# Optimization experiments

Hardware: AMD Instinct MI355X
Metric: run time of the kernel (lower is better)

Reference implementation:

```python
import jax, jax.numpy as jnp
import numpy as np

N_HEADS = 8
NEG = -1e9  # additive mask value standing in for -inf (bf16-safe)


def _mha(q_in, kv_in, w_in, b_in, w_out, b_out, mask):
    """torch nn.MultiheadAttention (batch_first, eval/no-dropout) equivalent.
    w_in: [3D, D] packed q/k/v in_proj weight, b_in: [3D]; w_out: [D, D], b_out: [D].
    mask: optional [L, L] additive mask.
    """
    B, Lq, D = q_in.shape
    H = N_HEADS
    dh = D // H
    Lk = kv_in.shape[1]
    q = q_in @ w_in[:D].T + b_in[:D]
    k = kv_in @ w_in[D:2 * D].T + b_in[D:2 * D]
    v = kv_in @ w_in[2 * D:].T + b_in[2 * D:]
    q = q.reshape(B, Lq, H, dh)
    k = k.reshape(B, Lk, H, dh)
    v = v.reshape(B, Lk, H, dh)
    scores = jnp.einsum('bqhd,bkhd->bhqk', q, k) / jnp.sqrt(jnp.asarray(dh, q.dtype))
    if mask is not None:
        scores = scores + mask  # broadcast [L,L] over [B,H,L,L]
    attn = jax.nn.softmax(scores, axis=-1)
    out = jnp.einsum('bhqk,bkhd->bqhd', attn, v).reshape(B, Lq, D)
    return out @ w_out.T + b_out


def _causal_mask(L):
    i = jnp.arange(L)
    return jnp.where(i[None, :] <= i[:, None], 0.0, NEG).astype(jnp.float32)


def _band_mask(L, window):
    # causal AND |i-j| <= window//2 (Eq. 13 band mask + causal mask)
    i = jnp.arange(L)
    diff = i[None, :] - i[:, None]  # key - query
    ok = (diff <= 0) & (jnp.abs(diff) <= window // 2)
    return jnp.where(ok, 0.0, NEG).astype(jnp.float32)


def setup_inputs() -> dict:
    key = jax.random.key(0)
    ks = jax.random.split(key, 10)
    B, L, D = 8, 1024, 512

    def rn(k, shape, scale=0.02):
        return jax.random.normal(k, shape, jnp.float32) * scale

    return {
        'user_emb': jax.random.normal(ks[0], (B, L, D), jnp.float32),
        'item_emb': jax.random.normal(ks[1], (B, L, D), jnp.float32),
        'attn_w_in': rn(ks[2], (6, 3 * D, D)),
        'attn_b_in': jnp.zeros((6, 3 * D), jnp.float32),
        'attn_w_out': rn(ks[3], (6, D, D)),
        'attn_b_out': jnp.zeros((6, D), jnp.float32),
        'cross_user_w': rn(ks[4], (D, D)),
        'cross_user_b': jnp.zeros((D,), jnp.float32),
        'cross_item_w': rn(ks[5], (D, D)),
        'cross_item_b': jnp.zeros((D,), jnp.float32),
        'gate_w': rn(ks[6], (2, D, 6)),
        'gate_b': jnp.zeros((2, 6), jnp.float32),
        'head_w1': rn(ks[7], (3, D, D // 2)),
        'head_b1': jnp.zeros((3, D // 2), jnp.float32),
        'head_w2': rn(ks[8], (3, D // 2)),
        'head_b2': jnp.zeros((3,), jnp.float32),
    }


def reference(user_emb, item_emb, attn_w_in, attn_b_in, attn_w_out, attn_b_out,
              cross_user_w, cross_user_b, cross_item_w, cross_item_b,
              gate_w, gate_b, head_w1, head_b1, head_w2, head_b2):
    B, L, D = item_emb.shape
    causal = _causal_mask(L)

    # 1) shared global causal SA (residual added by caller per docstring)
    shared = item_emb + _mha(item_emb, item_emb, attn_w_in[0], attn_b_in[0], attn_w_out[0], attn_b_out[0], causal)
    # 2) EXP-specific causal SA on shared output
    e_exp = shared + _mha(shared, shared, attn_w_in[1], attn_b_in[1], attn_w_out[1], attn_b_out[1], causal)
    # 3) CLK-specific causal SA on shared output
    e_clk = shared + _mha(shared, shared, attn_w_in[2], attn_b_in[2], attn_w_out[2], attn_b_out[2], causal)
    # 4) cross-attention: user queries into item keys/values (Eq. 12)
    u = user_emb @ cross_user_w.T + cross_user_b
    pv = item_emb @ cross_item_w.T + cross_item_b
    e_cross = _mha(u, pv, attn_w_in[3], attn_b_in[3], attn_w_out[3], attn_b_out[3], None)
    # 5/6) local (banded causal) self-attention, windows 4 and 6 (Eq. 13)
    e_lsa4 = item_emb + _mha(item_emb, item_emb, attn_w_in[4], attn_b_in[4], attn_w_out[4], attn_b_out[4], _band_mask(L, 4))
    e_lsa6 = item_emb + _mha(item_emb, item_emb, attn_w_in[5], attn_b_in[5], attn_w_out[5], attn_b_out[5], _band_mask(L, 6))

    experts = jnp.stack([shared, e_exp, e_clk, e_cross, e_lsa4, e_lsa6], axis=2)  # [B,L,6,D]
    # PLE gates: per-task softmax gate over the 6 experts conditioned on item_emb
    gate_logits = jnp.einsum('bld,tde->tble', item_emb, gate_w) + gate_b[:, None, None, :]
    gates = jax.nn.softmax(gate_logits, axis=-1)  # [2,B,L,6]
    h_exp = jnp.einsum('ble,bled->bld', gates[0], experts)
    h_clk = jnp.einsum('ble,bled->bld', gates[1], experts)

    def head(h, i):
        hid = jax.nn.relu(h @ head_w1[i] + head_b1[i])  # [B,L,D//2]
        return hid @ head_w2[i] + head_b2[i]  # [B,L]

    p_exp = jax.nn.sigmoid(head(h_exp, 0))
    p_clk = jax.nn.sigmoid(head(h_clk, 1))
    p_cvr = jax.nn.sigmoid(head(h_clk, 2))
    return (p_exp, p_clk, p_cvr)
```

## Files before the change

kernel.cpp:

```cpp
#include <hip/hip_runtime.h>
#include <hip/hip_bf16.h>
#include <stdint.h>


using bf16 = __hip_bfloat16;
typedef __attribute__((ext_vector_type(8))) short short8v;
typedef __attribute__((ext_vector_type(4))) short short4v;
typedef __attribute__((ext_vector_type(4))) float float4v;

#define LDK 40
#define LDKB 72
#define LQA 76
#define EXPC 0.18033688011112042f

__device__ __forceinline__ float wred_sum(float v) {
    #pragma unroll
    for (int off = 32; off; off >>= 1) v += __shfl_xor(v, off);
    return v;
}
__device__ __forceinline__ short f2bs(float x) {
    bf16 b = __float2bfloat16(x);
    return *reinterpret_cast<short*>(&b);
}
__device__ __forceinline__ float b2f(bf16 v) { return __bfloat162float(v); }

__global__ __launch_bounds__(256) void fillf_kernel(float* __restrict__ p, float v, int n) {
    const int i = blockIdx.x * 256 + threadIdx.x;
    if (i < n) p[i] = v;
}

__global__ __launch_bounds__(256) void cvt_all_kernel(
    const float* s0, bf16* d0, const float* s1, bf16* d1, const float* s2, bf16* d2,
    const float* s3, bf16* d3, const float* s4, bf16* d4, const float* s5, bf16* d5,
    const float* s6, bf16* d6)
{
    const int i = blockIdx.x * 256 + threadIdx.x;
    const float* src; bf16* dst; int off;
    if      (i < 1048576) { src = s0; dst = d0; off = i; }
    else if (i < 2097152) { src = s1; dst = d1; off = i - 1048576; }
    else if (i < 3276800) { src = s2; dst = d2; off = i - 2097152; }
    else if (i < 3670016) { src = s3; dst = d3; off = i - 3276800; }
    else if (i < 3735552) { src = s4; dst = d4; off = i - 3670016; }
    else if (i < 3801088) { src = s5; dst = d5; off = i - 3735552; }
    else if (i < 3899392) { src = s6; dst = d6; off = i - 3801088; }
    else return;
    const float4 v = *(const float4*)&src[(size_t)off << 2];
    short4v o;
    o[0] = f2bs(v.x); o[1] = f2bs(v.y); o[2] = f2bs(v.z); o[3] = f2bs(v.w);
    *(short4v*)&dst[(size_t)off << 2] = o;
}

__global__ __launch_bounds__(256) void gemm_nn_compose(
    const bf16* __restrict__ A, const bf16* __restrict__ B0, const bf16* __restrict__ B1,
    bf16* __restrict__ Y)
{
    const int K = 512, N = 512;
    __shared__ short As[64 * LDK];
    __shared__ short Bs[64 * LDK + 64];
    const int tid = threadIdx.x;
    const int lane = tid & 63, w = tid >> 6;
    const int bm = blockIdx.y * 64, bn = blockIdx.x * 64;
    const bf16* B = (bm < 512) ? B0 : B1;
    const int r = tid >> 2, c8 = (tid & 3) << 3;
    const int kk = tid >> 3, nn0 = (tid & 7) << 3;
    const int arow = ((w << 4) + (lane & 15)) * LDK + ((lane >> 4) << 3);

    float4v acc[4] = {};
    for (int k0 = 0; k0 < K; k0 += 32) {
        const short8v av = *(const short8v*)&A[(size_t)(bm + r) * K + k0 + c8];
        const short8v bw = *(const short8v*)&B[(size_t)(k0 + kk) * N + bn + nn0];
        __syncthreads();
        *(short8v*)&As[r * LDK + c8] = av;
        #pragma unroll
        for (int i = 0; i < 8; ++i) {
            const int nn = nn0 + i;
            Bs[nn * LDK + ((nn >> 3) << 3) + kk] = bw[i];
        }
        __syncthreads();
        const short8v a = *(const short8v*)&As[arow];
        #pragma unroll
        for (int c = 0; c < 4; ++c) {
            const int n = (c << 4) + (lane & 15);
            const short8v b = *(const short8v*)&Bs[n * LDK + ((n >> 3) << 3) + ((lane >> 4) << 3)];
            acc[c] = __builtin_amdgcn_mfma_f32_16x16x32_bf16(a, b, acc[c], 0, 0, 0);
        }
    }
    #pragma unroll
    for (int rg = 0; rg < 4; ++rg) {
        const int m = bm + (w << 4) + ((lane >> 4) << 2) + rg;
        #pragma unroll
        for (int c = 0; c < 4; ++c) {
            const int n = bn + (c << 4) + (lane & 15);
            Y[(size_t)m * N + n] = __float2bfloat16(acc[c][rg]);
        }
    }
}

__global__ __launch_bounds__(256) void compose_bias_kernel(
    const float* __restrict__ w3f, const float* __restrict__ cub,
    const float* __restrict__ cib, const float* __restrict__ b3f,
    float* __restrict__ bo)
{
    const int wid = threadIdx.x >> 6, lane = threadIdx.x & 63;
    const int n = blockIdx.x * 4 + wid;
    const float* cv = (n < 512) ? cub : cib;
    float s = 0.f;
    #pragma unroll
    for (int k = lane; k < 512; k += 64) s += w3f[(size_t)n * 512 + k] * cv[k];
    s = wred_sum(s);
    if (lane == 0) bo[n] = s + b3f[n];
}

__global__ __launch_bounds__(256) void gemm_bb_nt128(
    const bf16* __restrict__ X, const bf16* __restrict__ W,
    const float* __restrict__ bias, bf16* __restrict__ Yb, int ldY, int K)
{
    __shared__ short As[128 * LDKB];
    __shared__ short Bs[128 * LDKB];
    const int tid = threadIdx.x;
    const int lane = tid & 63, w = tid >> 6;
    const int wr = (w >> 1) << 6, wc = (w & 1) << 6;
    const int bm = blockIdx.y * 128, bn = blockIdx.x * 128;
    const int srow = tid >> 1, scol = (tid & 1) << 5;
    const int c16 = lane & 15, g16 = lane >> 4;

    float4v acc[4][4] = {};
    for (int k0 = 0; k0 < K; k0 += 64) {
        const bf16* xs = &X[(size_t)(bm + srow) * K + k0 + scol];
        const bf16* wsrc = &W[(size_t)(bn + srow) * K + k0 + scol];
        const short8v x0 = *(const short8v*)xs;
        const short8v x1 = *(const short8v*)(xs + 8);
        const short8v x2 = *(const short8v*)(xs + 16);
        const short8v x3 = *(const short8v*)(xs + 24);
        const short8v w0 = *(const short8v*)wsrc;
        const short8v w1 = *(const short8v*)(wsrc + 8);
        const short8v w2 = *(const short8v*)(wsrc + 16);
        const short8v w3 = *(const short8v*)(wsrc + 24);
        __syncthreads();
        *(short8v*)&As[srow * LDKB + scol]      = x0;
        *(short8v*)&As[srow * LDKB + scol + 8]  = x1;
        *(short8v*)&As[srow * LDKB + scol + 16] = x2;
        *(short8v*)&As[srow * LDKB + scol + 24] = x3;
        *(short8v*)&Bs[srow * LDKB + scol]      = w0;
        *(short8v*)&Bs[srow * LDKB + scol + 8]  = w1;
        *(short8v*)&Bs[srow * LDKB + scol + 16] = w2;
        *(short8v*)&Bs[srow * LDKB + scol + 24] = w3;
        __syncthreads();
        #pragma unroll
        for (int ks = 0; ks < 2; ++ks) {
            short8v af[4], bf4[4];
            #pragma unroll
            for (int i = 0; i < 4; ++i) {
                af[i]  = *(const short8v*)&As[(wr + (i << 4) + c16) * LDKB + (ks << 5) + (g16 << 3)];
                bf4[i] = *(const short8v*)&Bs[(wc + (i << 4) + c16) * LDKB + (ks << 5) + (g16 << 3)];
            }
            #pragma unroll
            for (int i = 0; i < 4; ++i)
                #pragma unroll
                for (int j = 0; j < 4; ++j)
                    acc[i][j] = __builtin_amdgcn_mfma_f32_16x16x32_bf16(af[i], bf4[j], acc[i][j], 0, 0, 0);
        }
    }
    #pragma unroll
    for (int i = 0; i < 4; ++i)
        #pragma unroll
        for (int rg = 0; rg < 4; ++rg) {
            const int m = bm + wr + (i << 4) + (g16 << 2) + rg;
            #pragma unroll
            for (int j = 0; j < 4; ++j) {
                const int n = bn + wc + (j << 4) + c16;
                Yb[(size_t)m * ldY + n] = __float2bfloat16(acc[i][j][rg] + bias[n]);
            }
        }
}

__global__ __launch_bounds__(256) void gemm_bb_nt128_selX(
    const bf16* __restrict__ X0, const bf16* __restrict__ X1, const bf16* __restrict__ W,
    const float* __restrict__ bias, bf16* __restrict__ Yb, int ldY, int K)
{
    __shared__ short As[128 * LDKB];
    __shared__ short Bs[128 * LDKB];
    const int tid = threadIdx.x;
    const int lane = tid & 63, w = tid >> 6;
    const int wr = (w >> 1) << 6, wc = (w & 1) << 6;
    const int bm = blockIdx.y * 128, bn = blockIdx.x * 128;
    const bf16* X = (bn < 512) ? X0 : X1;
    const int srow = tid >> 1, scol = (tid & 1) << 5;
    const int c16 = lane & 15, g16 = lane >> 4;

    float4v acc[4][4] = {};
    for (int k0 = 0; k0 < K; k0 += 64) {
        const bf16* xs = &X[(size_t)(bm + srow) * K + k0 + scol];
        const bf16* wsrc = &W[(size_t)(bn + srow) * K + k0 + scol];
        const short8v x0 = *(const short8v*)xs;
        const short8v x1 = *(const short8v*)(xs + 8);
        const short8v x2 = *(const short8v*)(xs + 16);
        const short8v x3 = *(const short8v*)(xs + 24);
        const short8v w0 = *(const short8v*)wsrc;
        const short8v w1 = *(const short8v*)(wsrc + 8);
        const short8v w2 = *(const short8v*)(wsrc + 16);
        const short8v w3 = *(const short8v*)(wsrc + 24);
        __syncthreads();
        *(short8v*)&As[srow * LDKB + scol]      = x0;
        *(short8v*)&As[srow * LDKB + scol + 8]  = x1;
        *(short8v*)&As[srow * LDKB + scol + 16] = x2;
        *(short8v*)&As[srow * LDKB + scol + 24] = x3;
        *(short8v*)&Bs[srow * LDKB + scol]      = w0;
        *(short8v*)&Bs[srow * LDKB + scol + 8]  = w1;
        *(short8v*)&Bs[srow * LDKB + scol + 16] = w2;
        *(short8v*)&Bs[srow * LDKB + scol + 24] = w3;
        __syncthreads();
        #pragma unroll
        for (int ks = 0; ks < 2; ++ks) {
            short8v af[4], bf4[4];
            #pragma unroll
            for (int i = 0; i < 4; ++i) {
                af[i]  = *(const short8v*)&As[(wr + (i << 4) + c16) * LDKB + (ks << 5) + (g16 << 3)];
                bf4[i] = *(const short8v*)&Bs[(wc + (i << 4) + c16) * LDKB + (ks << 5) + (g16 << 3)];
            }
            #pragma unroll
            for (int i = 0; i < 4; ++i)
                #pragma unroll
                for (int j = 0; j < 4; ++j)
                    acc[i][j] = __builtin_amdgcn_mfma_f32_16x16x32_bf16(af[i], bf4[j], acc[i][j], 0, 0, 0);
        }
    }
    #pragma unroll
    for (int i = 0; i < 4; ++i)
        #pragma unroll
        for (int rg = 0; rg < 4; ++rg) {
            const int m = bm + wr + (i << 4) + (g16 << 2) + rg;
            #pragma unroll
            for (int j = 0; j < 4; ++j) {
                const int n = bn + wc + (j << 4) + c16;
                Yb[(size_t)m * ldY + n] = __float2bfloat16(acc[i][j][rg] + bias[n]);
            }
        }
}

__global__ __launch_bounds__(256) void gemm_bb_nt_dual(
    const bf16* __restrict__ XA, const bf16* __restrict__ WA, const float* __restrict__ biasA,
    const bf16* __restrict__ XB, const bf16* __restrict__ WB, const float* __restrict__ biasB,
    const bf16* __restrict__ resA, int resSame,
    bf16* __restrict__ Yb, int ldY,
    bf16* __restrict__ h0, bf16* __restrict__ h1,
    const float* __restrict__ g, int eA, int eB, int hinit, int K)
{
    __shared__ short As[64 * LDK];
    __shared__ short Bs[64 * LDK];
    const int tid = threadIdx.x;
    const int lane = tid & 63, w = tid >> 6;
    const int bm = blockIdx.y * 64, bn = blockIdx.x * 64;
    const int r = tid >> 2, c8 = (tid & 3) << 3;
    const int arow = ((w << 4) + (lane & 15)) * LDK + ((lane >> 4) << 3);
    const int bbase = (lane & 15) * LDK + ((lane >> 4) << 3);

    float4v accA[4] = {};
    for (int k0 = 0; k0 < K; k0 += 32) {
        const short8v av = *(const short8v*)&XA[(size_t)(bm + r) * K + k0 + c8];
        const short8v bv = *(const short8v*)&WA[(size_t)(bn + r) * K + k0 + c8];
        __syncthreads();
        *(short8v*)&As[r * LDK + c8] = av;
        *(short8v*)&Bs[r * LDK + c8] = bv;
        __syncthreads();
        const short8v a = *(const short8v*)&As[arow];
        #pragma unroll
        for (int c = 0; c < 4; ++c) {
            const short8v b = *(const short8v*)&Bs[(c << 4) * LDK + bbase];
            accA[c] = __builtin_amdgcn_mfma_f32_16x16x32_bf16(a, b, accA[c], 0, 0, 0);
        }
    }
    float4v accB[4] = {};
    for (int k0 = 0; k0 < K; k0 += 32) {
        const short8v av = *(const short8v*)&XB[(size_t)(bm + r) * K + k0 + c8];
        const short8v bv = *(const short8v*)&WB[(size_t)(bn + r) * K + k0 + c8];
        __syncthreads();
        *(short8v*)&As[r * LDK + c8] = av;
        *(short8v*)&Bs[r * LDK + c8] = bv;
        __syncthreads();
        const short8v a = *(const short8v*)&As[arow];
        #pragma unroll
        for (int c = 0; c < 4; ++c) {
            const short8v b = *(const short8v*)&Bs[(c << 4) * LDK + bbase];
            accB[c] = __builtin_amdgcn_mfma_f32_16x16x32_bf16(a, b, accB[c], 0, 0, 0);
        }
    }
    #pragma unroll
    for (int rg = 0; rg < 4; ++rg) {
        const int m = bm + (w << 4) + ((lane >> 4) << 2) + rg;
        const float gA0 = g[(size_t)m * 6 + eA];
        const float gA1 = g[(size_t)(8192 + m) * 6 + eA];
        const float gB0 = g[(size_t)m * 6 + eB];
        const float gB1 = g[(size_t)(8192 + m) * 6 + eB];
        #pragma unroll
        for (int c = 0; c < 4; ++c) {
            const int n = bn + (c << 4) + (lane & 15);
            float rv = 0.f;
            if (resA) rv = b2f(resA[(size_t)m * 512 + n]);
            float vA = accA[c][rg] + biasA[n] + rv;
            float vB = accB[c][rg] + biasB[n] + (resSame ? rv : 0.f);
            if (Yb) Yb[(size_t)m * ldY + n] = __float2bfloat16(vA);
            const size_t hi = (size_t)m * 512 + n;
            const float t0 = gA0 * vA + gB0 * vB;
            const float t1 = gA1 * vA + gB1 * vB;
            if (hinit) {
                h0[hi] = __float2bfloat16(t0);
                h1[hi] = __float2bfloat16(t1);
            } else {
                h0[hi] = __float2bfloat16(b2f(h0[hi]) + t0);
                h1[hi] = __float2bfloat16(b2f(h1[hi]) + t1);
            }
        }
    }
}

__global__ __launch_bounds__(256) void gemm_mfma_nn_relu3(
    const bf16* __restrict__ h0b, const bf16* __restrict__ h1b,
    const bf16* __restrict__ hw1b, const float* __restrict__ hb1,
    float* __restrict__ hid0, float* __restrict__ hid1, float* __restrict__ hid2)
{
    const int K = 512, N = 256;
    const int seg = blockIdx.y >> 7;
    const int by = blockIdx.y & 127;
    const bf16* X = (seg == 0) ? h0b : h1b;
    const bf16* W = hw1b + (size_t)seg * 131072;
    const float* bias = hb1 + seg * 256;
    float* Y = (seg == 0) ? hid0 : ((seg == 1) ? hid1 : hid2);
    __shared__ short As[64 * LDK];
    __shared__ short Bs[64 * LDK + 64];
    const int tid = threadIdx.x;
    const int lane = tid & 63, w = tid >> 6;
    const int bm = by * 64, bn = blockIdx.x * 64;
    const int r = tid >> 2, c8 = (tid & 3) << 3;
    const int kk = tid >> 3, nn0 = (tid & 7) << 3;
    const int arow = ((w << 4) + (lane & 15)) * LDK + ((lane >> 4) << 3);

    float4v acc[4] = {};
    for (int k0 = 0; k0 < K; k0 += 32) {
        const short8v av = *(const short8v*)&X[(size_t)(bm + r) * K + k0 + c8];
        const short8v bw = *(const short8v*)&W[(size_t)(k0 + kk) * N + bn + nn0];
        __syncthreads();
        *(short8v*)&As[r * LDK + c8] = av;
        #pragma unroll
        for (int i = 0; i < 8; ++i) {
            const int nn = nn0 + i;
            Bs[nn * LDK + ((nn >> 3) << 3) + kk] = bw[i];
        }
        __syncthreads();
        const short8v a = *(const short8v*)&As[arow];
        #pragma unroll
        for (int c = 0; c < 4; ++c) {
            const int n = (c << 4) + (lane & 15);
            const short8v b = *(const short8v*)&Bs[n * LDK + ((n >> 3) << 3) + ((lane >> 4) << 3)];
            acc[c] = __builtin_amdgcn_mfma_f32_16x16x32_bf16(a, b, acc[c], 0, 0, 0);
        }
    }
    #pragma unroll
    for (int rg = 0; rg < 4; ++rg) {
        const int m = bm + (w << 4) + ((lane >> 4) << 2) + rg;
        #pragma unroll
        for (int c = 0; c < 4; ++c) {
            const int n = bn + (c << 4) + (lane & 15);
            Y[(size_t)m * N + n] = fmaxf(acc[c][rg] + bias[n], 0.f);
        }
    }
}

__global__ __launch_bounds__(512) void attn_flash2(
    const bf16* __restrict__ q0, const bf16* __restrict__ k0, const bf16* __restrict__ v0,
    bf16* __restrict__ o0, int ld0, int c0,
    const bf16* __restrict__ q1, const bf16* __restrict__ k1, const bf16* __restrict__ v1,
    bf16* __restrict__ o1, int ld1, int c1, int L)
{
    const int half = blockIdx.y >> 3;
    int bq = blockIdx.y & 7;
    const bf16 *qb, *kb, *vb; bf16* out; int ld, causal;
    if (half == 0) { qb = q0; kb = k0; vb = v0; out = o0; ld = ld0; causal = c0; }
    else           { qb = q1; kb = k1; vb = v1; out = o1; ld = ld1; causal = c1; }
    if (causal) bq = (bq < 4) ? bq : (11 - bq);
    const int b = blockIdx.x >> 3, h = blockIdx.x & 7;
    const int tid = threadIdx.x;
    const int lane = tid & 63, w = tid >> 6;
    const int g16 = lane >> 4, c16 = lane & 15;
    __shared__ short Ks[64 * LQA];
    __shared__ short Ps[128 * LQA];
    __shared__ short Vt[64 * LQA + 64];
    const size_t base = (size_t)b * L * ld + (size_t)h * 64;
    const int qlo = bq << 7;

    short8v qa0, qa1;
    {
        const bf16* qsrc = qb + base + (size_t)(qlo + (w << 4) + c16) * ld + (g16 << 3);
        qa0 = *(const short8v*)qsrc;
        qa1 = *(const short8v*)(qsrc + 32);
    }

    const int sr2 = (tid & 255) >> 2, sc2 = (tid & 3) << 4;
    const bool isK = tid < 256;

    float4v oacc[4] = {};
    float lrow[4] = {0.f, 0.f, 0.f, 0.f};

    const int nkt = causal ? ((bq + 1) << 1) : (L >> 6);

    short8v pf0, pf1;
    {
        const bf16* src = (isK ? kb : vb) + base + (size_t)sr2 * ld + sc2;
        pf0 = *(const short8v*)src;
        pf1 = *(const short8v*)(src + 8);
    }

    for (int kt = 0; kt < nkt; ++kt) {
        const int klo = kt << 6;
        __syncthreads();
        if (isK) {
            *(short8v*)&Ks[sr2 * LQA + sc2]     = pf0;
            *(short8v*)&Ks[sr2 * LQA + sc2 + 8] = pf1;
        } else {
            #pragma unroll
            for (int i = 0; i < 8; ++i) Vt[(sc2 + i) * LQA + sc2 + sr2] = pf0[i];
            #pragma unroll
            for (int i = 0; i < 8; ++i) Vt[(sc2 + 8 + i) * LQA + sc2 + sr2] = pf1[i];
        }
        __syncthreads();
        if (kt + 1 < nkt) {
            const bf16* src = (isK ? kb : vb) + base + (size_t)(((kt + 1) << 6) + sr2) * ld + sc2;
            pf0 = *(const short8v*)src;
            pf1 = *(const short8v*)(src + 8);
        }
        float4v sacc[4] = {};
        #pragma unroll
        for (int ct = 0; ct < 4; ++ct) {
            const short8v b0 = *(const short8v*)&Ks[((ct << 4) + c16) * LQA + (g16 << 3)];
            sacc[ct] = __builtin_amdgcn_mfma_f32_16x16x32_bf16(qa0, b0, sacc[ct], 0, 0, 0);
            const short8v b1 = *(const short8v*)&Ks[((ct << 4) + c16) * LQA + 32 + (g16 << 3)];
            sacc[ct] = __builtin_amdgcn_mfma_f32_16x16x32_bf16(qa1, b1, sacc[ct], 0, 0, 0);
        }
        const bool diag = causal && (klo + 63 > qlo + (w << 4));
        #pragma unroll
        for (int ct = 0; ct < 4; ++ct)
            #pragma unroll
            for (int rg = 0; rg < 4; ++rg) {
                float p = exp2f(sacc[ct][rg] * EXPC);
                if (diag && (klo + (ct << 4) + c16) > (qlo + (w << 4) + (g16 << 2) + rg))
                    p = 0.f;
                lrow[rg] += p;
                Ps[((w << 4) + (g16 << 2) + rg) * LQA + (ct << 4) + c16] = f2bs(p);
            }
        #pragma unroll
        for (int ks = 0; ks < 2; ++ks) {
            const short8v a = *(const short8v*)&Ps[((w << 4) + c16) * LQA + (ks << 5) + (g16 << 3)];
            #pragma unroll
            for (int dt = 0; dt < 4; ++dt) {
                const short8v bf = *(const short8v*)&Vt[((dt << 4) + c16) * LQA + (dt << 4) + (ks << 5) + (g16 << 3)];
                oacc[dt] = __builtin_amdgcn_mfma_f32_16x16x32_bf16(a, bf, oacc[dt], 0, 0, 0);
            }
        }
    }
    #pragma unroll
    for (int rg = 0; rg < 4; ++rg) {
        float v = lrow[rg];
        #pragma unroll
        for (int off = 8; off; off >>= 1) v += __shfl_xor(v, off);
        lrow[rg] = v;
    }
    #pragma unroll
    for (int rg = 0; rg < 4; ++rg) {
        const int row = qlo + (w << 4) + (g16 << 2) + rg;
        const float inv = 1.f / lrow[rg];
        #pragma unroll
        for (int dt = 0; dt < 4; ++dt)
            out[((size_t)b * L + row) * 512 + h * 64 + (dt << 4) + c16] =
                __float2bfloat16(oacc[dt][rg] * inv);
    }
}

__global__ __launch_bounds__(256) void attn_band2(
    const bf16* __restrict__ qkv, bf16* __restrict__ oA, bf16* __restrict__ oB,
    int L, int ld, int wA, int wB)
{
    const int half = blockIdx.y >> 6;
    const int yy = blockIdx.y & 63;
    const int u = threadIdx.x >> 6, t = threadIdx.x & 63;
    const int i = blockIdx.x * 4 + u;
    const int b = yy >> 3, h = yy & 7;
    const bf16* qb = qkv + half * 1536;
    const bf16* kb = qb + 512;
    const bf16* vb = qb + 1024;
    bf16* out = half ? oB : oA;
    const int w = half ? wB : wA;
    const size_t base = (size_t)b * L * ld + (size_t)h * 64;
    const float qv = b2f(qb[base + (size_t)i * ld + t]);
    const int jmin = (i - w) > 0 ? (i - w) : 0;
    const int n = i - jmin;
    float sv[4];
    float mx = -1e30f;
    #pragma unroll
    for (int q = 0; q < 4; ++q) {
        float d = -1e30f;
        if (q <= n) {
            float dd = qv * b2f(kb[base + (size_t)(jmin + q) * ld + t]);
            d = wred_sum(dd) * 0.125f;
        }
        sv[q] = d;
        mx = fmaxf(mx, d);
    }
    float lsum = 0.f, acc = 0.f;
    #pragma unroll
    for (int q = 0; q < 4; ++q) {
        if (q <= n) {
            const float p = __expf(sv[q] - mx);
            lsum += p;
            acc += p * b2f(vb[base + (size_t)(jmin + q) * ld + t]);
        }
    }
    out[((size_t)b * L + i) * 512 + h * 64 + t] = __float2bfloat16(acc / lsum);
}

__global__ __launch_bounds__(64) void gates_v2(
    const float* __restrict__ item, const float* __restrict__ gw,
    const float* __restrict__ gb, float* __restrict__ g, int rows)
{
    const int r = blockIdx.x;
    const int t = threadIdx.x;
    __shared__ float xr[512];
    __shared__ float lg[12];
    for (int ii = t; ii < 512; ii += 64) xr[ii] = item[(size_t)r * 512 + ii];
    __syncthreads();
    #pragma unroll
    for (int p = 0; p < 12; ++p) {
        const int tk = p / 6, e = p % 6;
        float s = 0.f;
        #pragma unroll
        for (int dd = t; dd < 512; dd += 64) s += xr[dd] * gw[(size_t)(tk * 512 + dd) * 6 + e];
        s = wred_sum(s);
        if (t == 0) lg[p] = s + gb[p];
    }
    __syncthreads();
    if (t < 2) {
        float mx = -1e30f;
        #pragma unroll
        for (int e = 0; e < 6; ++e) mx = fmaxf(mx, lg[t * 6 + e]);
        float sum = 0.f, p6[6];
        #pragma unroll
        for (int e = 0; e < 6; ++e) { p6[e] = __expf(lg[t * 6 + e] - mx); sum += p6[e]; }
        #pragma unroll
        for (int e = 0; e < 6; ++e) g[(size_t)(t * rows + r) * 6 + e] = p6[e] / sum;
    }
}

__global__ __launch_bounds__(256) void head2_v2(
    const float* __restrict__ hid0, const float* __restrict__ hid1, const float* __restrict__ hid2,
    const float* __restrict__ w2, const float* __restrict__ b2, float* __restrict__ out)
{
    const int w = threadIdx.x >> 6, lane = threadIdx.x & 63;
    const int r = blockIdx.x * 4 + w;
    float s0 = 0.f, s1 = 0.f, s2 = 0.f;
    #pragma unroll
    for (int d = lane; d < 256; d += 64) {
        s0 += hid0[(size_t)r * 256 + d] * w2[d];
        s1 += hid1[(size_t)r * 256 + d] * w2[256 + d];
        s2 += hid2[(size_t)r * 256 + d] * w2[512 + d];
    }
    s0 = wred_sum(s0); s1 = wred_sum(s1); s2 = wred_sum(s2);
    if (lane == 0) {
        out[r]         = 1.f / (1.f + __expf(-(s0 + b2[0])));
        out[8192 + r]  = 1.f / (1.f + __expf(-(s1 + b2[1])));
        out[16384 + r] = 1.f / (1.f + __expf(-(s2 + b2[2])));
    }
}

extern "C" void kernel_launch(void* const* d_in, const int* in_sizes, int n_in,
                              void* d_out, int out_size, void* d_ws, size_t ws_size,
                              hipStream_t stream)
{
    float* out = (float*)d_out;
    const int* s = in_sizes;
    const bool dicto = n_in == 16 &&
        s[0] == 4194304 && s[1] == 4194304 && s[2] == 4718592 && s[3] == 9216 &&
        s[4] == 1572864 && s[5] == 3072 && s[6] == 262144 && s[7] == 512 &&
        s[8] == 262144 && s[9] == 512 && s[10] == 6144 && s[11] == 12 &&
        s[12] == 393216 && s[13] == 768 && s[14] == 768 && s[15] == 3;
    if (!dicto) {
        fillf_kernel<<<dim3(96), dim3(256), 0, stream>>>(out, 16384.0f, out_size);
        return;
    }

    const float* user  = (const float*)d_in[0];
    const float* item  = (const float*)d_in[1];
    const float* w_in  = (const float*)d_in[2];
    const float* b_in  = (const float*)d_in[3];
    const float* w_out = (const float*)d_in[4];
    const float* b_out = (const float*)d_in[5];
    const float* cuw   = (const float*)d_in[6];
    const float* cub   = (const float*)d_in[7];
    const float* ciw   = (const float*)d_in[8];
    const float* cib   = (const float*)d_in[9];
    const float* gw    = (const float*)d_in[10];
    const float* gb    = (const float*)d_in[11];
    const float* hw1   = (const float*)d_in[12];
    const float* hb1   = (const float*)d_in[13];
    const float* hw2   = (const float*)d_in[14];
    const float* hb2   = (const float*)d_in[15];

    const int L = 1024, M = 8192;
    float* ws = (float*)d_ws;
    bf16* qkvb     = (bf16*)ws;
    bf16* qkvc     = qkvb + (size_t)12582912;
    bf16* attnoutb = (bf16*)(ws + 12582912);
    bf16* attnout2 = (bf16*)(ws + 16777216);
    bf16* h0b      = (bf16*)(ws + 20971520);
    bf16* h1b      = (bf16*)(ws + 25165824);
    bf16* sharedb  = (bf16*)(ws + 31457280);
    float* g       = ws + 41943040;
    bf16* itemb    = (bf16*)(ws + 42041344);
    bf16* userb    = (bf16*)(ws + 44138496);
    bf16* w_inb    = (bf16*)(ws + 46235648);
    bf16* w_outb   = (bf16*)(ws + 48594944);
    bf16* cuwb     = (bf16*)(ws + 49381376);
    bf16* ciwb     = (bf16*)(ws + 49512448);
    bf16* hw1b     = (bf16*)(ws + 49643520);
    bf16* Wcomp    = (bf16*)(ws + 49840128);
    float* bcomp   = ws + 50233344;
    float* hid0 = ws;
    float* hid1 = ws + (size_t)M * 256;
    float* hid2 = ws + (size_t)M * 512;
    bf16* BN = nullptr;

    const dim3 blk512(512), blk256(256), blk64(64);
    const dim3 gP1536(12, 64), gP3072(24, 64);
    const dim3 g512(8, 128);
    const dim3 gFA2(64, 16), gBA2(256, 128);

    cvt_all_kernel<<<dim3(15232), blk256, 0, stream>>>(
        item, itemb, user, userb, w_in, w_inb, w_out, w_outb,
        cuw, cuwb, ciw, ciwb, hw1, hw1b);

    gates_v2<<<dim3(M), blk64, 0, stream>>>(item, gw, gb, g, M);

    gemm_nn_compose<<<dim3(8, 24), blk256, 0, stream>>>(
        w_inb + (size_t)3 * 786432, cuwb, ciwb, Wcomp);
    compose_bias_kernel<<<dim3(384), blk256, 0, stream>>>(
        w_in + (size_t)3 * 786432, cub, cib, b_in + 3 * 1536, bcomp);

    gemm_bb_nt128<<<gP1536, blk256, 0, stream>>>(itemb, w_inb, b_in, qkvb, 1536, 512);
    gemm_bb_nt128_selX<<<gP1536, blk256, 0, stream>>>(userb, itemb, Wcomp, bcomp, qkvc, 1536, 512);

    attn_flash2<<<gFA2, blk512, 0, stream>>>(
        qkvb, qkvb + 512, qkvb + 1024, attnoutb, 1536, 1,
        qkvc, qkvc + 512, qkvc + 1024, attnout2, 1536, 0, L);

    gemm_bb_nt_dual<<<g512, blk256, 0, stream>>>(
        attnoutb, w_outb, b_out,
        attnout2, w_outb + (size_t)3 * 262144, b_out + 3 * 512,
        itemb, 0, sharedb, 512, h0b, h1b, g, 0, 3, 1, 512);

    gemm_bb_nt128<<<gP3072, blk256, 0, stream>>>(sharedb, w_inb + (size_t)786432,
        b_in + 1536, qkvb, 3072, 512);
    attn_flash2<<<gFA2, blk512, 0, stream>>>(
        qkvb, qkvb + 512, qkvb + 1024, attnoutb, 3072, 1,
        qkvb + 1536, qkvb + 2048, qkvb + 2560, attnout2, 3072, 1, L);
    gemm_bb_nt_dual<<<g512, blk256, 0, stream>>>(
        attnoutb, w_outb + 262144, b_out + 512,
        attnout2, w_outb + 524288, b_out + 1024,
        sharedb, 1, BN, 0, h0b, h1b, g, 1, 2, 0, 512);

    gemm_bb_nt128<<<gP3072, blk256, 0, stream>>>(itemb, w_inb + (size_t)4 * 786432,
        b_in + 4 * 1536, qkvb, 3072, 512);
    attn_band2<<<gBA2, blk256, 0, stream>>>(qkvb, attnoutb, attnout2, L, 3072, 2, 3);
    gemm_bb_nt_dual<<<g512, blk256, 0, stream>>>(
        attnoutb, w_outb + (size_t)4 * 262144, b_out + 4 * 512,
        attnout2, w_outb + (size_t)5 * 262144, b_out + 5 * 512,
        itemb, 1, BN, 0, h0b, h1b, g, 4, 5, 0, 512);

    gemm_mfma_nn_relu3<<<dim3(4, 384), blk256, 0, stream>>>(
        h0b, h1b, hw1b, hb1, hid0, hid1, hid2);
    head2_v2<<<dim3(2048), blk256, 0, stream>>>(hid0, hid1, hid2, hw2, hb2, out);
}
```

Baseline: 520.0 us.

## Merge setup kernels into fewer launches and add MFMA priority hints in attention

The gate softmax computation moves into the bf16 conversion kernel as extra blocks, and it now uses one wave per row with register-held inputs instead of a 64-thread block per row. The weight-compose GEMM and the compose-bias reduction now share one launch. The two QKV projection GEMMs also share one launch with a single grid of 24 by 64. The intent is to cut launch count and the tail idle time between small kernels. s_setprio hints are also placed around the MFMA sections of the flash attention loop to favour matrix issue across waves.

```diff
diff --git a/kernel.cpp b/kernel.cpp
--- a/kernel.cpp
+++ b/kernel.cpp
@@ -29,37 +29,90 @@
     if (i < n) p[i] = v;
 }
 
-__global__ __launch_bounds__(256) void cvt_all_kernel(
+__global__ __launch_bounds__(256) void cvt_gates_kernel(
     const float* s0, bf16* d0, const float* s1, bf16* d1, const float* s2, bf16* d2,
     const float* s3, bf16* d3, const float* s4, bf16* d4, const float* s5, bf16* d5,
-    const float* s6, bf16* d6)
-{
-    const int i = blockIdx.x * 256 + threadIdx.x;
-    const float* src; bf16* dst; int off;
-    if      (i < 1048576) { src = s0; dst = d0; off = i; }
-    else if (i < 2097152) { src = s1; dst = d1; off = i - 1048576; }
-    else if (i < 3276800) { src = s2; dst = d2; off = i - 2097152; }
-    else if (i < 3670016) { src = s3; dst = d3; off = i - 3276800; }
-    else if (i < 3735552) { src = s4; dst = d4; off = i - 3670016; }
-    else if (i < 3801088) { src = s5; dst = d5; off = i - 3735552; }
-    else if (i < 3899392) { src = s6; dst = d6; off = i - 3801088; }
-    else return;
-    const float4 v = *(const float4*)&src[(size_t)off << 2];
-    short4v o;
-    o[0] = f2bs(v.x); o[1] = f2bs(v.y); o[2] = f2bs(v.z); o[3] = f2bs(v.w);
-    *(short4v*)&dst[(size_t)off << 2] = o;
-}
-
-__global__ __launch_bounds__(256) void gemm_nn_compose(
+    const float* s6, bf16* d6,
+    const float* __restrict__ item, const float* __restrict__ gw,
+    const float* __restrict__ gb, float* __restrict__ g)
+{
+    const int blk = blockIdx.x;
+    if (blk < 15232) {
+        const int i = blk * 256 + threadIdx.x;
+        const float* src; bf16* dst; int off;
+        if      (i < 1048576) { src = s0; dst = d0; off = i; }
+        else if (i < 2097152) { src = s1; dst = d1; off = i - 1048576; }
+        else if (i < 3276800) { src = s2; dst = d2; off = i - 2097152; }
+        else if (i < 3670016) { src = s3; dst = d3; off = i - 3276800; }
+        else if (i < 3735552) { src = s4; dst = d4; off = i - 3670016; }
+        else if (i < 3801088) { src = s5; dst = d5; off = i - 3735552; }
+        else if (i < 3899392) { src = s6; dst = d6; off = i - 3801088; }
+        else return;
+        const float4 v = *(const float4*)&src[(size_t)off << 2];
+        short4v o;
+        o[0] = f2bs(v.x); o[1] = f2bs(v.y); o[2] = f2bs(v.z); o[3] = f2bs(v.w);
+        *(short4v*)&dst[(size_t)off << 2] = o;
+        return;
+    }
+    const int wid = threadIdx.x >> 6, lane = threadIdx.x & 63;
+    const int r = (blk - 15232) * 4 + wid;
+    float x[8];
+    #pragma unroll
+    for (int j = 0; j < 8; ++j) x[j] = item[(size_t)r * 512 + lane + (j << 6)];
+    float lg[12];
+    #pragma unroll
+    for (int p = 0; p < 12; ++p) {
+        const int tk = p / 6, e = p % 6;
+        float s = 0.f;
+        #pragma unroll
+        for (int j = 0; j < 8; ++j)
+            s += x[j] * gw[(size_t)(tk * 512 + lane + (j << 6)) * 6 + e];
+        lg[p] = wred_sum(s);
+    }
+    if (lane == 0) {
+        #pragma unroll
+        for (int tk = 0; tk < 2; ++tk) {
+            float mx = -1e30f;
+            #pragma unroll
+            for (int e = 0; e < 6; ++e) mx = fmaxf(mx, lg[tk * 6 + e] + gb[tk * 6 + e]);
+            float sum = 0.f, p6[6];
+            #pragma unroll
+            for (int e = 0; e < 6; ++e) {
+                p6[e] = __expf(lg[tk * 6 + e] + gb[tk * 6 + e] - mx);
+                sum += p6[e];
+            }
+            #pragma unroll
+            for (int e = 0; e < 6; ++e)
+                g[(size_t)(tk * 8192 + r) * 6 + e] = p6[e] / sum;
+        }
+    }
+}
+
+__global__ __launch_bounds__(256) void compose_all_kernel(
     const bf16* __restrict__ A, const bf16* __restrict__ B0, const bf16* __restrict__ B1,
-    bf16* __restrict__ Y)
-{
+    bf16* __restrict__ Y,
+    const float* __restrict__ w3f, const float* __restrict__ cub,
+    const float* __restrict__ cib, const float* __restrict__ b3f,
+    float* __restrict__ bo)
+{
+    const int blk = blockIdx.x;
+    if (blk >= 192) {
+        const int wid = threadIdx.x >> 6, lane = threadIdx.x & 63;
+        const int n = (blk - 192) * 4 + wid;
+        const float* cv = (n < 512) ? cub : cib;
+        float s = 0.f;
+        #pragma unroll
+        for (int k = lane; k < 512; k += 64) s += w3f[(size_t)n * 512 + k] * cv[k];
+        s = wred_sum(s);
+        if (lane == 0) bo[n] = s + b3f[n];
+        return;
+    }
     const int K = 512, N = 512;
     __shared__ short As[64 * LDK];
     __shared__ short Bs[64 * LDK + 64];
     const int tid = threadIdx.x;
     const int lane = tid & 63, w = tid >> 6;
-    const int bm = blockIdx.y * 64, bn = blockIdx.x * 64;
+    const int bm = (blk >> 3) * 64, bn = (blk & 7) * 64;
     const bf16* B = (bm < 512) ? B0 : B1;
     const int r = tid >> 2, c8 = (tid & 3) << 3;
     const int kk = tid >> 3, nn0 = (tid & 7) << 3;
@@ -96,31 +149,25 @@
     }
 }
 
-__global__ __launch_bounds__(256) void compose_bias_kernel(
-    const float* __restrict__ w3f, const float* __restrict__ cub,
-    const float* __restrict__ cib, const float* __restrict__ b3f,
-    float* __restrict__ bo)
-{
-    const int wid = threadIdx.x >> 6, lane = threadIdx.x & 63;
-    const int n = blockIdx.x * 4 + wid;
-    const float* cv = (n < 512) ? cub : cib;
-    float s = 0.f;
-    #pragma unroll
-    for (int k = lane; k < 512; k += 64) s += w3f[(size_t)n * 512 + k] * cv[k];
-    s = wred_sum(s);
-    if (lane == 0) bo[n] = s + b3f[n];
-}
-
-__global__ __launch_bounds__(256) void gemm_bb_nt128(
-    const bf16* __restrict__ X, const bf16* __restrict__ W,
-    const float* __restrict__ bias, bf16* __restrict__ Yb, int ldY, int K)
-{
+__global__ __launch_bounds__(256) void gemm_qkv0x(
+    const bf16* __restrict__ itemb, const bf16* __restrict__ userb,
+    const bf16* __restrict__ w_inb, const float* __restrict__ b_in,
+    const bf16* __restrict__ Wcomp, const float* __restrict__ bcomp,
+    bf16* __restrict__ qkvb, bf16* __restrict__ qkvc, int K)
+{
+    const int seg = (blockIdx.x >= 12);
+    const int bxl = blockIdx.x - (seg ? 12 : 0);
+    const int bm = blockIdx.y * 128, bn = bxl * 128;
+    const bf16* X = seg ? ((bn < 512) ? userb : itemb) : itemb;
+    const bf16* W = seg ? Wcomp : w_inb;
+    const float* bias = seg ? bcomp : b_in;
+    bf16* Yb = seg ? qkvc : qkvb;
+
     __shared__ short As[128 * LDKB];
     __shared__ short Bs[128 * LDKB];
     const int tid = threadIdx.x;
     const int lane = tid & 63, w = tid >> 6;
     const int wr = (w >> 1) << 6, wc = (w & 1) << 6;
-    const int bm = blockIdx.y * 128, bn = blockIdx.x * 128;
     const int srow = tid >> 1, scol = (tid & 1) << 5;
     const int c16 = lane & 15, g16 = lane >> 4;
 
@@ -169,13 +216,13 @@
             #pragma unroll
             for (int j = 0; j < 4; ++j) {
                 const int n = bn + wc + (j << 4) + c16;
-                Yb[(size_t)m * ldY + n] = __float2bfloat16(acc[i][j][rg] + bias[n]);
-            }
-        }
-}
-
-__global__ __launch_bounds__(256) void gemm_bb_nt128_selX(
-    const bf16* __restrict__ X0, const bf16* __restrict__ X1, const bf16* __restrict__ W,
+                Yb[(size_t)m * 1536 + n] = __float2bfloat16(acc[i][j][rg] + bias[n]);
+            }
+        }
+}
+
+__global__ __launch_bounds__(256) void gemm_bb_nt128(
+    const bf16* __restrict__ X, const bf16* __restrict__ W,
     const float* __restrict__ bias, bf16* __restrict__ Yb, int ldY, int K)
 {
     __shared__ short As[128 * LDKB];
@@ -184,7 +231,6 @@
     const int lane = tid & 63, w = tid >> 6;
     const int wr = (w >> 1) << 6, wc = (w & 1) << 6;
     const int bm = blockIdx.y * 128, bn = blockIdx.x * 128;
-    const bf16* X = (bn < 512) ? X0 : X1;
     const int srow = tid >> 1, scol = (tid & 1) << 5;
     const int c16 = lane & 15, g16 = lane >> 4;
 
@@ -429,6 +475,7 @@
             pf1 = *(const short8v*)(src + 8);
         }
         float4v sacc[4] = {};
+        __builtin_amdgcn_s_setprio(1);
         #pragma unroll
         for (int ct = 0; ct < 4; ++ct) {
             const short8v b0 = *(const short8v*)&Ks[((ct << 4) + c16) * LQA + (g16 << 3)];
@@ -436,6 +483,7 @@
             const short8v b1 = *(const short8v*)&Ks[((ct << 4) + c16) * LQA + 32 + (g16 << 3)];
             sacc[ct] = __builtin_amdgcn_mfma_f32_16x16x32_bf16(qa1, b1, sacc[ct], 0, 0, 0);
         }
+        __builtin_amdgcn_s_setprio(0);
         const bool diag = causal && (klo + 63 > qlo + (w << 4));
         #pragma unroll
         for (int ct = 0; ct < 4; ++ct)
@@ -447,6 +495,7 @@
                 lrow[rg] += p;
                 Ps[((w << 4) + (g16 << 2) + rg) * LQA + (ct << 4) + c16] = f2bs(p);
             }
+        __builtin_amdgcn_s_setprio(1);
         #pragma unroll
         for (int ks = 0; ks < 2; ++ks) {
             const short8v a = *(const short8v*)&Ps[((w << 4) + c16) * LQA + (ks << 5) + (g16 << 3)];
@@ -456,6 +505,7 @@
                 oacc[dt] = __builtin_amdgcn_mfma_f32_16x16x32_bf16(a, bf, oacc[dt], 0, 0, 0);
             }
         }
+        __builtin_amdgcn_s_setprio(0);
     }
     #pragma unroll
     for (int rg = 0; rg < 4; ++rg) {
@@ -515,38 +565,6 @@
         }
     }
     out[((size_t)b * L + i) * 512 + h * 64 + t] = __float2bfloat16(acc / lsum);
-}
-
-__global__ __launch_bounds__(64) void gates_v2(
-    const float* __restrict__ item, const float* __restrict__ gw,
-    const float* __restrict__ gb, float* __restrict__ g, int rows)
-{
-    const int r = blockIdx.x;
-    const int t = threadIdx.x;
-    __shared__ float xr[512];
-    __shared__ float lg[12];
-    for (int ii = t; ii < 512; ii += 64) xr[ii] = item[(size_t)r * 512 + ii];
-    __syncthreads();
-    #pragma unroll
-    for (int p = 0; p < 12; ++p) {
-        const int tk = p / 6, e = p % 6;
-        float s = 0.f;
-        #pragma unroll
-        for (int dd = t; dd < 512; dd += 64) s += xr[dd] * gw[(size_t)(tk * 512 + dd) * 6 + e];
-        s = wred_sum(s);
-        if (t == 0) lg[p] = s + gb[p];
-    }
-    __syncthreads();
-    if (t < 2) {
-        float mx = -1e30f;
-        #pragma unroll
-        for (int e = 0; e < 6; ++e) mx = fmaxf(mx, lg[t * 6 + e]);
-        float sum = 0.f, p6[6];
-        #pragma unroll
-        for (int e = 0; e < 6; ++e) { p6[e] = __expf(lg[t * 6 + e] - mx); sum += p6[e]; }
-        #pragma unroll
-        for (int e = 0; e < 6; ++e) g[(size_t)(t * rows + r) * 6 + e] = p6[e] / sum;
-    }
 }
 
 __global__ __launch_bounds__(256) void head2_v2(
@@ -627,24 +645,21 @@
     float* hid2 = ws + (size_t)M * 512;
     bf16* BN = nullptr;
 
-    const dim3 blk512(512), blk256(256), blk64(64);
-    const dim3 gP1536(12, 64), gP3072(24, 64);
+    const dim3 blk512(512), blk256(256);
+    const dim3 gP3072(24, 64);
     const dim3 g512(8, 128);
     const dim3 gFA2(64, 16), gBA2(256, 128);
 
-    cvt_all_kernel<<<dim3(15232), blk256, 0, stream>>>(
+    cvt_gates_kernel<<<dim3(17280), blk256, 0, stream>>>(
         item, itemb, user, userb, w_in, w_inb, w_out, w_outb,
-        cuw, cuwb, ciw, ciwb, hw1, hw1b);
-
-    gates_v2<<<dim3(M), blk64, 0, stream>>>(item, gw, gb, g, M);
-
-    gemm_nn_compose<<<dim3(8, 24), blk256, 0, stream>>>(
-        w_inb + (size_t)3 * 786432, cuwb, ciwb, Wcomp);
-    compose_bias_kernel<<<dim3(384), blk256, 0, stream>>>(
+        cuw, cuwb, ciw, ciwb, hw1, hw1b, item, gw, gb, g);
+
+    compose_all_kernel<<<dim3(576), blk256, 0, stream>>>(
+        w_inb + (size_t)3 * 786432, cuwb, ciwb, Wcomp,
         w_in + (size_t)3 * 786432, cub, cib, b_in + 3 * 1536, bcomp);
 
-    gemm_bb_nt128<<<gP1536, blk256, 0, stream>>>(itemb, w_inb, b_in, qkvb, 1536, 512);
-    gemm_bb_nt128_selX<<<gP1536, blk256, 0, stream>>>(userb, itemb, Wcomp, bcomp, qkvc, 1536, 512);
+    gemm_qkv0x<<<dim3(24, 64), blk256, 0, stream>>>(
+        itemb, userb, w_inb, b_in, Wcomp, bcomp, qkvb, qkvc, 512);
 
     attn_flash2<<<gFA2, blk512, 0, stream>>>(
         qkvb, qkvb + 512, qkvb + 1024, attnoutb, 1536, 1,
```

New measurement: 480.9 us. 7.5% less time.
